# Performance work log

Hardware: AMD Instinct MI355X
Metric: run time of the kernel (lower is better)

Reference implementation:

```python
import jax, jax.numpy as jnp
import numpy as np
import math

EMBED_DIM = 2048
NUM_HEADS = 32
NUM_KV_HEADS = 8
HEAD_DIM = EMBED_DIM // NUM_HEADS  # 64
N_REP = NUM_HEADS // NUM_KV_HEADS  # 4
BATCH = 2
SEQ = 2048


def _rope_tables(seq_len, head_dim):
    # standard RoPE tables matching rotate_half convention (frequencies tiled twice)
    inv_freq = 1.0 / (10000.0 ** (np.arange(0, head_dim, 2, dtype=np.float32) / head_dim))
    t = np.arange(seq_len, dtype=np.float32)
    freqs = np.outer(t, inv_freq)                      # (seq, head_dim/2)
    emb = np.concatenate([freqs, freqs], axis=-1)      # (seq, head_dim)
    return jnp.asarray(np.cos(emb)), jnp.asarray(np.sin(emb))


def setup_inputs() -> dict:
    key = jax.random.key(0)
    ks = jax.random.split(key, 6)
    scale = 1.0 / math.sqrt(EMBED_DIM)
    x = jax.random.normal(ks[0], (BATCH, SEQ, EMBED_DIM), dtype=jnp.float32)
    wq = jax.random.normal(ks[1], (EMBED_DIM, EMBED_DIM), dtype=jnp.float32) * scale
    wk = jax.random.normal(ks[2], (NUM_KV_HEADS * HEAD_DIM, EMBED_DIM), dtype=jnp.float32) * scale
    wv = jax.random.normal(ks[3], (NUM_KV_HEADS * HEAD_DIM, EMBED_DIM), dtype=jnp.float32) * scale
    wo = jax.random.normal(ks[4], (EMBED_DIM, EMBED_DIM), dtype=jnp.float32) * scale
    freqs_cos, freqs_sin = _rope_tables(SEQ, HEAD_DIM)
    return {"x": x, "freqs_cos": freqs_cos, "freqs_sin": freqs_sin,
            "wq": wq, "wk": wk, "wv": wv, "wo": wo}


def _rotate_half(t):
    h = t.shape[-1] // 2
    return jnp.concatenate([-t[..., h:], t[..., :h]], axis=-1)


def reference(x, freqs_cos, freqs_sin, wq, wk, wv, wo):
    b, s, _ = x.shape
    # QKV projections (Linear with weight (out,in): y = x @ W^T)
    xq = (x @ wq.T).reshape(b, s, NUM_HEADS, HEAD_DIM).transpose(0, 2, 1, 3)     # (b,H,s,d)
    xk = (x @ wk.T).reshape(b, s, NUM_KV_HEADS, HEAD_DIM).transpose(0, 2, 1, 3)  # (b,Hkv,s,d)
    xv = (x @ wv.T).reshape(b, s, NUM_KV_HEADS, HEAD_DIM).transpose(0, 2, 1, 3)
    # RoPE: cos/sin (s,d) broadcast over (b,h,s,d)
    xq = xq * freqs_cos + _rotate_half(xq) * freqs_sin
    xk = xk * freqs_cos + _rotate_half(xk) * freqs_sin
    # GQA: repeat_interleave kv heads to match q heads
    xk = jnp.repeat(xk, N_REP, axis=1)  # (b,H,s,d)
    xv = jnp.repeat(xv, N_REP, axis=1)
    scores = jnp.einsum('bhqd,bhkd->bhqk', xq, xk) / math.sqrt(HEAD_DIM)
    causal = jnp.tril(jnp.ones((s, s), dtype=bool))
    scores = jnp.where(causal, scores, jnp.float32(-1e30))
    attn = jax.nn.softmax(scores, axis=-1)
    out = jnp.einsum('bhqk,bhkd->bhqd', attn, xv)        # (b,H,s,d)
    out = out.transpose(0, 2, 1, 3).reshape(b, s, EMBED_DIM)
    return out @ wo.T
```

## Files before the change

### kernel.cpp

```cpp
#include <hip/hip_runtime.h>

#define BATCH 2
#define SEQ 2048
#define EMBED 2048
#define NHEADS 32
#define NKV 8
#define HDIM 64
#define QKV_LD 3072

typedef __attribute__((ext_vector_type(8))) short short8;
typedef __attribute__((ext_vector_type(4))) float f32x4;

__device__ inline ushort f2bf(float f) {
  union { float f; unsigned u; } v{f};
  unsigned r = v.u + 0x7FFF + ((v.u >> 16) & 1);
  return (ushort)(r >> 16);
}
__device__ inline float bf2f(ushort u) {
  union { unsigned u; float f; } v{((unsigned)u) << 16};
  return v.f;
}
__device__ inline unsigned fbits(float f) {
  union { float f; unsigned u; } v{f};
  return v.u;
}

__device__ inline void gload16(const ushort* g, ushort* l) {
  __builtin_amdgcn_global_load_lds(
      (const __attribute__((address_space(1))) unsigned*)g,
      (__attribute__((address_space(3))) unsigned*)l, 16, 0, 0);
}

__global__ void f32_to_bf16_kernel(const float* __restrict__ in,
                                   ushort* __restrict__ out, int n) {
  int i = (blockIdx.x * blockDim.x + threadIdx.x) * 4;
  if (i >= n) return;
  float4 v = *(const float4*)(in + i);
  ushort4 o;
  o.x = f2bf(v.x); o.y = f2bf(v.y); o.z = f2bf(v.z); o.w = f2bf(v.w);
  *(ushort4*)(out + i) = o;
}

template <typename OutT>
__global__ __launch_bounds__(256) void gemm_bf16(const ushort* __restrict__ A,
                                                 const ushort* __restrict__ B,
                                                 OutT* __restrict__ C,
                                                 int M, int N, int K) {
  __shared__ ushort As[128][32];
  __shared__ ushort Bs[128][32];
  const int tid = threadIdx.x;
  const int lane = tid & 63, wave = tid >> 6;
  const int quad = lane >> 4, l16 = lane & 15;
  const int m0 = blockIdx.y * 128, n0 = blockIdx.x * 128;
  const int wm = (wave >> 1) * 64, wn = (wave & 1) * 64;
  const int srow = lane >> 2, skq = (lane & 3) * 8;

  f32x4 acc[4][4] = {};
  for (int k0 = 0; k0 < K; k0 += 32) {
    const ushort* ga = A + (size_t)(m0 + wave * 32 + srow) * K + k0 + skq;
    const ushort* gb = B + (size_t)(n0 + wave * 32 + srow) * K + k0 + skq;
    __syncthreads();
    gload16(ga, &As[wave * 32][0]);
    gload16(ga + (size_t)16 * K, &As[wave * 32 + 16][0]);
    gload16(gb, &Bs[wave * 32][0]);
    gload16(gb + (size_t)16 * K, &Bs[wave * 32 + 16][0]);
    __syncthreads();
    short8 af[4], bf[4];
#pragma unroll
    for (int i = 0; i < 4; i++) af[i] = *(short8*)&As[wm + i * 16 + l16][quad * 8];
#pragma unroll
    for (int j = 0; j < 4; j++) bf[j] = *(short8*)&Bs[wn + j * 16 + l16][quad * 8];
#pragma unroll
    for (int i = 0; i < 4; i++)
#pragma unroll
      for (int j = 0; j < 4; j++)
        acc[i][j] = __builtin_amdgcn_mfma_f32_16x16x32_bf16(af[i], bf[j], acc[i][j], 0, 0, 0);
  }
#pragma unroll
  for (int i = 0; i < 4; i++) {
#pragma unroll
    for (int r = 0; r < 4; r++) {
      size_t rg = (size_t)(m0 + wm + i * 16 + quad * 4 + r);
#pragma unroll
      for (int j = 0; j < 4; j++) {
        float v = acc[i][j][r];
        int cg = n0 + wn + j * 16 + l16;
        if constexpr (sizeof(OutT) == 2)
          C[rg * N + cg] = f2bf(v);
        else
          C[rg * N + cg] = v;
      }
    }
  }
}

__global__ void rope_qk(ushort* __restrict__ t, const float* __restrict__ fc,
                        const float* __restrict__ fs, int total) {
  int idx = blockIdx.x * blockDim.x + threadIdx.x;
  if (idx >= total) return;
  int i = idx & 31;
  int hh = (idx >> 5) % 40;
  int tok = idx / (32 * 40);
  int s = tok & (SEQ - 1);
  float scale = (hh < 32) ? 0.125f : 1.0f;
  ushort* p = t + (size_t)tok * QKV_LD + hh * 64;
  float x0 = bf2f(p[i]), x1 = bf2f(p[i + 32]);
  float c0 = fc[s * HDIM + i], s0 = fs[s * HDIM + i];
  float c1 = fc[s * HDIM + i + 32], s1 = fs[s * HDIM + i + 32];
  p[i] = f2bf((x0 * c0 - x1 * s0) * scale);
  p[i + 32] = f2bf((x1 * c1 + x0 * s1) * scale);
}

__global__ __launch_bounds__(256) void attn_mfma(const ushort* __restrict__ QKV,
                                                 ushort* __restrict__ O) {
  __shared__ ushort Ks[64][72];
  __shared__ ushort Vt[64][72];
  __shared__ ushort Pw[4][16][72];
  const int tid = threadIdx.x;
  const int lane = tid & 63, wave = tid >> 6;
  const int quad = lane >> 4, l16 = lane & 15;
  const int bh = blockIdx.y;
  const int b = bh >> 5, h = bh & 31, kh = h >> 2;
  const int p = blockIdx.x;
  const int qt[2] = {p, 31 - p};
  const int ntiles = 32 - p;

  short8 qf[2][2];
#pragma unroll
  for (int u = 0; u < 2; u++)
#pragma unroll
    for (int c = 0; c < 2; c++)
      qf[u][c] = *(const short8*)(QKV +
          (size_t)(b * SEQ + qt[u] * 64 + wave * 16 + l16) * QKV_LD +
          h * HDIM + c * 32 + quad * 8);

  f32x4 o[2][4] = {};
  float m[2] = {-INFINITY, -INFINITY}, l[2] = {0.f, 0.f};

  const ushort* Kbase = QKV + (size_t)b * SEQ * QKV_LD + 2048 + kh * HDIM;
  const ushort* Vbase = Kbase + 512;
  const int kp = tid & 31, dg = tid >> 5;
  const int relrow = wave * 16 + l16;

  for (int t = 0; t < ntiles; t++) {
    const int k0 = t * 64;
    __syncthreads();
    {
      const float4* kpp = (const float4*)(Kbase + (size_t)(k0 + lane) * QKV_LD + wave * 16);
      float4 kv0 = kpp[0], kv1 = kpp[1];
      const uint4* va4 = (const uint4*)(Vbase + (size_t)(k0 + 2 * kp) * QKV_LD + dg * 8);
      const uint4* vb4 = (const uint4*)(Vbase + (size_t)(k0 + 2 * kp + 1) * QKV_LD + dg * 8);
      uint4 va = va4[0], vb = vb4[0];
      *(float4*)&Ks[lane][wave * 16] = kv0;
      *(float4*)&Ks[lane][wave * 16 + 8] = kv1;
      const unsigned* vaw = (const unsigned*)&va;
      const unsigned* vbw = (const unsigned*)&vb;
#pragma unroll
      for (int j = 0; j < 8; j++) {
        unsigned pk = (j & 1)
            ? __builtin_amdgcn_perm(vbw[j >> 1], vaw[j >> 1], 0x07060302)
            : __builtin_amdgcn_perm(vbw[j >> 1], vaw[j >> 1], 0x05040100);
        *(unsigned*)&Vt[dg * 8 + j][2 * kp] = pk;
      }
    }
    __syncthreads();

#pragma unroll
    for (int u = 0; u < 2; u++) {
      const int diag = qt[u];
      if (t > diag) continue;

      f32x4 s[4];
#pragma unroll
      for (int nt = 0; nt < 4; nt++) {
        short8 kf0 = *(short8*)&Ks[nt * 16 + l16][quad * 8];
        short8 kf1 = *(short8*)&Ks[nt * 16 + l16][32 + quad * 8];
        f32x4 z = {};
        z = __builtin_amdgcn_mfma_f32_16x16x32_bf16(kf0, qf[u][0], z, 0, 0, 0);
        s[nt] = __builtin_amdgcn_mfma_f32_16x16x32_bf16(kf1, qf[u][1], z, 0, 0, 0);
      }

      if (t == diag) {
#pragma unroll
        for (int nt = 0; nt < 4; nt++)
#pragma unroll
          for (int r = 0; r < 4; r++)
            if (nt * 16 + quad * 4 + r > relrow) s[nt][r] = -INFINITY;
      }

      float mx = -INFINITY;
#pragma unroll
      for (int nt = 0; nt < 4; nt++)
#pragma unroll
        for (int r = 0; r < 4; r++) mx = fmaxf(mx, s[nt][r]);
      mx = fmaxf(mx, __shfl_xor(mx, 16));
      mx = fmaxf(mx, __shfl_xor(mx, 32));
      float mnew = fmaxf(m[u], mx);
      float al = __expf(m[u] - mnew);
      m[u] = mnew;

      float pv[16];
      float psum = 0.f;
#pragma unroll
      for (int nt = 0; nt < 4; nt++)
#pragma unroll
        for (int r = 0; r < 4; r++) {
          float pe = __expf(s[nt][r] - mnew);
          pv[nt * 4 + r] = pe;
          psum += pe;
        }
      psum += __shfl_xor(psum, 16);
      psum += __shfl_xor(psum, 32);
      l[u] = l[u] * al + psum;
#pragma unroll
      for (int dt = 0; dt < 4; dt++)
#pragma unroll
        for (int r = 0; r < 4; r++) o[u][dt][r] *= al;

#pragma unroll
      for (int nt = 0; nt < 4; nt++) {
        unsigned lo = __builtin_amdgcn_perm(fbits(pv[nt * 4 + 1]), fbits(pv[nt * 4 + 0]), 0x07060302);
        unsigned hi = __builtin_amdgcn_perm(fbits(pv[nt * 4 + 3]), fbits(pv[nt * 4 + 2]), 0x07060302);
        uint2 pk; pk.x = lo; pk.y = hi;
        *(uint2*)&Pw[wave][l16][nt * 16 + quad * 4] = pk;
      }
      short8 pf0 = *(short8*)&Pw[wave][l16][quad * 8];
      short8 pf1 = *(short8*)&Pw[wave][l16][32 + quad * 8];
#pragma unroll
      for (int dt = 0; dt < 4; dt++) {
        short8 vf0 = *(short8*)&Vt[dt * 16 + l16][quad * 8];
        short8 vf1 = *(short8*)&Vt[dt * 16 + l16][32 + quad * 8];
        o[u][dt] = __builtin_amdgcn_mfma_f32_16x16x32_bf16(vf0, pf0, o[u][dt], 0, 0, 0);
        o[u][dt] = __builtin_amdgcn_mfma_f32_16x16x32_bf16(vf1, pf1, o[u][dt], 0, 0, 0);
      }
    }
  }

#pragma unroll
  for (int u = 0; u < 2; u++) {
    float inv = 1.0f / l[u];
    size_t rowg = (size_t)(b * SEQ + qt[u] * 64 + wave * 16 + l16) * EMBED + h * HDIM;
#pragma unroll
    for (int dt = 0; dt < 4; dt++) {
      ushort q0 = f2bf(o[u][dt][0] * inv), q1 = f2bf(o[u][dt][1] * inv);
      ushort q2 = f2bf(o[u][dt][2] * inv), q3 = f2bf(o[u][dt][3] * inv);
      uint2 pk;
      pk.x = (unsigned)q0 | ((unsigned)q1 << 16);
      pk.y = (unsigned)q2 | ((unsigned)q3 << 16);
      *(uint2*)&O[rowg + dt * 16 + quad * 4] = pk;
    }
  }
}

extern "C" void kernel_launch(void* const* d_in, const int* in_sizes, int n_in,
                              void* d_out, int out_size, void* d_ws, size_t ws_size,
                              hipStream_t stream) {
  const float* x = (const float*)d_in[0];
  const float* fcos = (const float*)d_in[1];
  const float* fsin = (const float*)d_in[2];
  const float* wq = (const float*)d_in[3];
  const float* wk = (const float*)d_in[4];
  const float* wv = (const float*)d_in[5];
  const float* wo = (const float*)d_in[6];
  float* out = (float*)d_out;

  const int M = BATCH * SEQ;
  ushort* ws = (ushort*)d_ws;
  ushort* xb = ws;
  ushort* wqkv = xb + (size_t)M * EMBED;
  ushort* wob = wqkv + (size_t)QKV_LD * EMBED;
  ushort* QKVb = wob + (size_t)EMBED * EMBED;
  ushort* Ab = QKVb + (size_t)M * QKV_LD;

  dim3 blk(256);
  auto cvt = [&](const float* src, ushort* dst, size_t n) {
    f32_to_bf16_kernel<<<(n / 4 + 255) / 256, blk, 0, stream>>>(src, dst, (int)n);
  };
  cvt(x, xb, (size_t)M * EMBED);
  cvt(wq, wqkv, (size_t)EMBED * EMBED);
  cvt(wk, wqkv + (size_t)EMBED * EMBED, (size_t)512 * EMBED);
  cvt(wv, wqkv + (size_t)(EMBED + 512) * EMBED, (size_t)512 * EMBED);
  cvt(wo, wob, (size_t)EMBED * EMBED);

  gemm_bf16<ushort><<<dim3(QKV_LD / 128, M / 128), blk, 0, stream>>>(xb, wqkv, QKVb, M, QKV_LD, EMBED);

  {
    int tot = M * 40 * 32;
    rope_qk<<<(tot + 255) / 256, blk, 0, stream>>>(QKVb, fcos, fsin, tot);
  }

  attn_mfma<<<dim3(16, BATCH * NHEADS), blk, 0, stream>>>(QKVb, Ab);

  gemm_bf16<float><<<dim3(EMBED / 128, M / 128), blk, 0, stream>>>(Ab, wob, out, M, EMBED, EMBED);
}
```

Before: 345.0 us.

## Fuse conversion launches, vectorize RoPE, switch softmax to exp2 with folded log2e

Replaces the five separate fp32-to-bf16 conversion launches with one kernel that converts 8 elements per thread across all inputs. Vectorizes the RoPE kernel so each thread handles 8 pairs through 16-byte loads and stores. Folds log2(e) into the Q scale so attention can use the hardware exp2 instruction in place of __expf. This cuts launch overhead, narrow memory accesses and exponent cost, at the price of hardcoded offsets in the conversion kernel.

Measured after the change: 328.2 us. 1.05x faster.

```diff
diff --git a/kernel.cpp b/kernel.cpp
--- a/kernel.cpp
+++ b/kernel.cpp
@@ -7,9 +7,12 @@
 #define NKV 8
 #define HDIM 64
 #define QKV_LD 3072
+#define LOG2E 1.44269504088896f
 
 typedef __attribute__((ext_vector_type(8))) short short8;
 typedef __attribute__((ext_vector_type(4))) float f32x4;
+
+__device__ inline float hw_exp2(float x) { return __builtin_amdgcn_exp2f(x); }
 
 __device__ inline ushort f2bf(float f) {
   union { float f; unsigned u; } v{f};
@@ -31,14 +34,28 @@
       (__attribute__((address_space(3))) unsigned*)l, 16, 0, 0);
 }
 
-__global__ void f32_to_bf16_kernel(const float* __restrict__ in,
-                                   ushort* __restrict__ out, int n) {
-  int i = (blockIdx.x * blockDim.x + threadIdx.x) * 4;
-  if (i >= n) return;
-  float4 v = *(const float4*)(in + i);
-  ushort4 o;
-  o.x = f2bf(v.x); o.y = f2bf(v.y); o.z = f2bf(v.z); o.w = f2bf(v.w);
-  *(ushort4*)(out + i) = o;
+__global__ __launch_bounds__(256) void cvt_all(const float* __restrict__ x,
+                                               const float* __restrict__ wq,
+                                               const float* __restrict__ wk,
+                                               const float* __restrict__ wv,
+                                               const float* __restrict__ wo,
+                                               ushort* __restrict__ xb,
+                                               ushort* __restrict__ wqkv,
+                                               ushort* __restrict__ wob) {
+  size_t e = (size_t)(blockIdx.x * blockDim.x + threadIdx.x) * 8;
+  const float* src;
+  ushort* dst;
+  if (e < 8388608u) { src = x + e; dst = xb + e; }
+  else if (e < 12582912u) { size_t o = e - 8388608u; src = wq + o; dst = wqkv + o; }
+  else if (e < 13631488u) { size_t o = e - 12582912u; src = wk + o; dst = wqkv + 4194304u + o; }
+  else if (e < 14680064u) { size_t o = e - 13631488u; src = wv + o; dst = wqkv + 5242880u + o; }
+  else { size_t o = e - 14680064u; src = wo + o; dst = wob + o; }
+  float4 v0 = ((const float4*)src)[0];
+  float4 v1 = ((const float4*)src)[1];
+  union { uint4 v; ushort u[8]; } pk;
+  pk.u[0] = f2bf(v0.x); pk.u[1] = f2bf(v0.y); pk.u[2] = f2bf(v0.z); pk.u[3] = f2bf(v0.w);
+  pk.u[4] = f2bf(v1.x); pk.u[5] = f2bf(v1.y); pk.u[6] = f2bf(v1.z); pk.u[7] = f2bf(v1.w);
+  *(uint4*)dst = pk.v;
 }
 
 template <typename OutT>
@@ -94,21 +111,39 @@
   }
 }
 
-__global__ void rope_qk(ushort* __restrict__ t, const float* __restrict__ fc,
-                        const float* __restrict__ fs, int total) {
+__global__ __launch_bounds__(256) void rope_qk(ushort* __restrict__ t,
+                                               const float* __restrict__ fc,
+                                               const float* __restrict__ fs,
+                                               int total) {
   int idx = blockIdx.x * blockDim.x + threadIdx.x;
   if (idx >= total) return;
-  int i = idx & 31;
-  int hh = (idx >> 5) % 40;
-  int tok = idx / (32 * 40);
+  int g = idx & 3;
+  int hh = (idx >> 2) % 40;
+  int tok = idx / 160;
   int s = tok & (SEQ - 1);
-  float scale = (hh < 32) ? 0.125f : 1.0f;
-  ushort* p = t + (size_t)tok * QKV_LD + hh * 64;
-  float x0 = bf2f(p[i]), x1 = bf2f(p[i + 32]);
-  float c0 = fc[s * HDIM + i], s0 = fs[s * HDIM + i];
-  float c1 = fc[s * HDIM + i + 32], s1 = fs[s * HDIM + i + 32];
-  p[i] = f2bf((x0 * c0 - x1 * s0) * scale);
-  p[i + 32] = f2bf((x1 * c1 + x0 * s1) * scale);
+  float scale = (hh < 32) ? 0.125f * LOG2E : 1.0f;
+  ushort* p = t + (size_t)tok * QKV_LD + hh * 64 + g * 8;
+  union { uint4 v; ushort u[8]; } lo, hi, olo, ohi;
+  lo.v = *(const uint4*)p;
+  hi.v = *(const uint4*)(p + 32);
+  const float* fcb = fc + s * HDIM + g * 8;
+  const float* fsb = fs + s * HDIM + g * 8;
+  float4 c0a = ((const float4*)fcb)[0], c0b = ((const float4*)fcb)[1];
+  float4 s0a = ((const float4*)fsb)[0], s0b = ((const float4*)fsb)[1];
+  float4 c1a = ((const float4*)(fcb + 32))[0], c1b = ((const float4*)(fcb + 32))[1];
+  float4 s1a = ((const float4*)(fsb + 32))[0], s1b = ((const float4*)(fsb + 32))[1];
+  float cc0[8] = {c0a.x, c0a.y, c0a.z, c0a.w, c0b.x, c0b.y, c0b.z, c0b.w};
+  float ss0[8] = {s0a.x, s0a.y, s0a.z, s0a.w, s0b.x, s0b.y, s0b.z, s0b.w};
+  float cc1[8] = {c1a.x, c1a.y, c1a.z, c1a.w, c1b.x, c1b.y, c1b.z, c1b.w};
+  float ss1[8] = {s1a.x, s1a.y, s1a.z, s1a.w, s1b.x, s1b.y, s1b.z, s1b.w};
+#pragma unroll
+  for (int j = 0; j < 8; j++) {
+    float x0 = bf2f(lo.u[j]), x1 = bf2f(hi.u[j]);
+    olo.u[j] = f2bf((x0 * cc0[j] - x1 * ss0[j]) * scale);
+    ohi.u[j] = f2bf((x1 * cc1[j] + x0 * ss1[j]) * scale);
+  }
+  *(uint4*)p = olo.v;
+  *(uint4*)(p + 32) = ohi.v;
 }
 
 __global__ __launch_bounds__(256) void attn_mfma(const ushort* __restrict__ QKV,
@@ -196,7 +231,7 @@
       mx = fmaxf(mx, __shfl_xor(mx, 16));
       mx = fmaxf(mx, __shfl_xor(mx, 32));
       float mnew = fmaxf(m[u], mx);
-      float al = __expf(m[u] - mnew);
+      float al = hw_exp2(m[u] - mnew);
       m[u] = mnew;
 
       float pv[16];
@@ -205,7 +240,7 @@
       for (int nt = 0; nt < 4; nt++)
 #pragma unroll
         for (int r = 0; r < 4; r++) {
-          float pe = __expf(s[nt][r] - mnew);
+          float pe = hw_exp2(s[nt][r] - mnew);
           pv[nt * 4 + r] = pe;
           psum += pe;
         }
@@ -273,19 +308,12 @@
   ushort* Ab = QKVb + (size_t)M * QKV_LD;
 
   dim3 blk(256);
-  auto cvt = [&](const float* src, ushort* dst, size_t n) {
-    f32_to_bf16_kernel<<<(n / 4 + 255) / 256, blk, 0, stream>>>(src, dst, (int)n);
-  };
-  cvt(x, xb, (size_t)M * EMBED);
-  cvt(wq, wqkv, (size_t)EMBED * EMBED);
-  cvt(wk, wqkv + (size_t)EMBED * EMBED, (size_t)512 * EMBED);
-  cvt(wv, wqkv + (size_t)(EMBED + 512) * EMBED, (size_t)512 * EMBED);
-  cvt(wo, wob, (size_t)EMBED * EMBED);
+  cvt_all<<<9216, blk, 0, stream>>>(x, wq, wk, wv, wo, xb, wqkv, wob);
 
   gemm_bf16<ushort><<<dim3(QKV_LD / 128, M / 128), blk, 0, stream>>>(xb, wqkv, QKVb, M, QKV_LD, EMBED);
 
   {
-    int tot = M * 40 * 32;
+    int tot = M * 40 * 4;
     rope_qk<<<(tot + 255) / 256, blk, 0, stream>>>(QKVb, fcos, fsin, tot);
   }
 
```
